# Optimization experiments

Measured on AMD Instinct MI355X. Metric: run time of the kernel, lower is better.

The kernel has to match this reference:

```python
import jax, jax.numpy as jnp
import numpy as np

B, S, H = 2, 2048, 1024
NH, HD = 16, 64
WIN = 256
EPS = 1e-5


def _layernorm(x, g, b):
    # normalize over last dim (head_dim)
    m = jnp.mean(x, axis=-1, keepdims=True)
    v = jnp.mean((x - m) ** 2, axis=-1, keepdims=True)
    return (x - m) * jax.lax.rsqrt(v + EPS) * g + b


def setup_inputs() -> dict:
    key = jax.random.key(0)
    ks = jax.random.split(key, 6)
    scale = 1.0 / np.sqrt(2.0 * H)  # ~ xavier_uniform with gain 1/sqrt(2)
    inp = {
        "x": jax.random.normal(ks[0], (B, S, H), dtype=jnp.float32),
        "Wq": jax.random.normal(ks[1], (H, H), dtype=jnp.float32) * scale,
        "bq": jnp.zeros((H,), jnp.float32),
        "Wk": jax.random.normal(ks[2], (H, H), dtype=jnp.float32) * scale,
        "bk": jnp.zeros((H,), jnp.float32),
        "Wv": jax.random.normal(ks[3], (H, H), dtype=jnp.float32) * scale,
        "bv": jnp.zeros((H,), jnp.float32),
        "Wo": jax.random.normal(ks[4], (H, H), dtype=jnp.float32) * scale,
        "bo": jnp.zeros((H,), jnp.float32),
        "ln_q_w": jnp.ones((HD,), jnp.float32),
        "ln_q_b": jnp.zeros((HD,), jnp.float32),
        "ln_k_w": jnp.ones((HD,), jnp.float32),
        "ln_k_b": jnp.zeros((HD,), jnp.float32),
    }
    return inp


def reference(x, Wq, bq, Wk, bk, Wv, bv, Wo, bo, ln_q_w, ln_q_b, ln_k_w, ln_k_b):
    b, s, _ = x.shape
    # projections (torch Linear: x @ W.T + b)
    q = (x @ Wq.T + bq).reshape(b, s, NH, HD)
    k = (x @ Wk.T + bk).reshape(b, s, NH, HD)
    v = (x @ Wv.T + bv).reshape(b, s, NH, HD)
    # QK layernorm over head_dim
    q = _layernorm(q, ln_q_w, ln_q_b)
    k = _layernorm(k, ln_k_w, ln_k_b)
    # scores [b, h, s, s]
    scores = jnp.einsum("bqhd,bkhd->bhqk", q, k) / np.sqrt(HD).astype(np.float32)
    i = jnp.arange(s)[:, None]
    j = jnp.arange(s)[None, :]
    mask = (j <= i) & (i - j <= WIN)
    scores = jnp.where(mask[None, None], scores, -jnp.inf)
    probs = jax.nn.softmax(scores, axis=-1)
    out = jnp.einsum("bhqk,bkhd->bqhd", probs, v).reshape(b, s, NH * HD)
    return out @ Wo.T + bo
```

## Files before the change

### kernel.cpp

```cpp
#include <hip/hip_runtime.h>
#include <hip/hip_bf16.h>
#include <cstdint>

typedef __hip_bfloat16 bf16;
typedef __attribute__((ext_vector_type(8))) short s16x8;
typedef __attribute__((ext_vector_type(4))) float f32x4;

#define NB_B 2
#define NB_S 2048
#define NB_H 1024
#define NB_NH 16
#define NB_HD 64
#define NB_WIN 256
#define NTOK 4096

static __device__ __forceinline__ unsigned pack_bf16(float a, float b) {
    bf16 ta = __float2bfloat16(a), tb = __float2bfloat16(b);
    return (unsigned)*(unsigned short*)&ta | ((unsigned)*(unsigned short*)&tb << 16);
}
static __device__ __forceinline__ unsigned short bf16u(float a) {
    bf16 t = __float2bfloat16(a);
    return *(unsigned short*)&t;
}

#define VMCNT(n) asm volatile("s_waitcnt vmcnt(" #n ")" ::: "memory")
#define SBAR __builtin_amdgcn_s_barrier()
#define LGKM0 do { asm volatile("s_waitcnt lgkmcnt(0)" ::: "memory"); \
                   __builtin_amdgcn_sched_barrier(0); } while (0)

__global__ void k_castall(const float* __restrict__ x, const float* __restrict__ Wq,
                          const float* __restrict__ Wk, const float* __restrict__ Wv,
                          const float* __restrict__ Wo,
                          bf16* __restrict__ xb, bf16* __restrict__ wqkvb,
                          bf16* __restrict__ wob) {
    int idx = blockIdx.x * blockDim.x + threadIdx.x;
    const float* in; bf16* out; int i;
    if (idx < 1048576)        { in = x;  out = xb;              i = idx * 4; }
    else if (idx < 1310720)   { in = Wq; out = wqkvb;           i = (idx - 1048576) * 4; }
    else if (idx < 1572864)   { in = Wk; out = wqkvb + 1048576; i = (idx - 1310720) * 4; }
    else if (idx < 1835008)   { in = Wv; out = wqkvb + 2097152; i = (idx - 1572864) * 4; }
    else                      { in = Wo; out = wob;             i = (idx - 1835008) * 4; }
    const float4 v = *(const float4*)(in + i);
    ushort4 u;
    u.x = bf16u(v.x); u.y = bf16u(v.y); u.z = bf16u(v.z); u.w = bf16u(v.w);
    *(ushort4*)((unsigned short*)out + i) = u;
}

#define GQ_STAGE(AD, BD, KT)                                                         \
    do {                                                                             \
        _Pragma("unroll")                                                            \
        for (int it_ = 0; it_ < 2; ++it_) {                                          \
            int c_ = it_ * 256 + tid;                                                \
            int row_ = c_ >> 2, pc_ = c_ & 3;                                        \
            int col_ = (pc_ ^ ((row_ >> 1) & 3)) << 3;                               \
            __builtin_amdgcn_global_load_lds(                                        \
                (const __attribute__((address_space(1))) void*)(Ap + (size_t)(m0 + row_) * 1024 + (KT) + col_), \
                (__attribute__((address_space(3))) void*)((AD) + c_ * 8), 16, 0, 0); \
            __builtin_amdgcn_global_load_lds(                                        \
                (const __attribute__((address_space(1))) void*)(Bp + (size_t)(n0 + row_) * 1024 + (KT) + col_), \
                (__attribute__((address_space(3))) void*)((BD) + c_ * 8), 16, 0, 0); \
        }                                                                            \
        __builtin_amdgcn_sched_barrier(0);                                           \
    } while (0)

#define GQ_COMPUTE(AS, BS)                                                           \
    do {                                                                             \
        const int chv_ = (g ^ ((q >> 1) & 3)) << 3;                                  \
        s16x8 af_[4], bf_[4];                                                        \
        _Pragma("unroll")                                                            \
        for (int mi_ = 0; mi_ < 4; ++mi_)                                            \
            af_[mi_] = *(const s16x8*)&(AS)[(wr * 64 + mi_ * 16 + q) * 32 + chv_];   \
        _Pragma("unroll")                                                            \
        for (int ni_ = 0; ni_ < 4; ++ni_)                                            \
            bf_[ni_] = *(const s16x8*)&(BS)[(wc * 64 + ni_ * 16 + q) * 32 + chv_];   \
        LGKM0;                                                                       \
        __builtin_amdgcn_s_setprio(1);                                               \
        _Pragma("unroll")                                                            \
        for (int mi_ = 0; mi_ < 4; ++mi_)                                            \
            _Pragma("unroll")                                                        \
            for (int ni_ = 0; ni_ < 4; ++ni_)                                        \
                acc[mi_][ni_] = __builtin_amdgcn_mfma_f32_16x16x32_bf16(             \
                    af_[mi_], bf_[ni_], acc[mi_][ni_], 0, 0, 0);                     \
        __builtin_amdgcn_s_setprio(0);                                               \
    } while (0)

#define GQ_MAINLOOP(NT)                                                              \
    GQ_STAGE(Asb + 0 * ABUF, Bsb + 0 * BBUF, 0);                                     \
    GQ_STAGE(Asb + 1 * ABUF, Bsb + 1 * BBUF, 32);                                    \
    {                                                                                \
        int bc_ = 0, bs_ = 2;                                                        \
        for (int t_ = 0; t_ < (NT) - 2; ++t_) {                                      \
            GQ_STAGE(Asb + bs_ * ABUF, Bsb + bs_ * BBUF, (t_ + 2) * 32);             \
            VMCNT(8); SBAR;                                                          \
            GQ_COMPUTE(Asb + bc_ * ABUF, Bsb + bc_ * BBUF);                          \
            SBAR;                                                                    \
            bc_ = (bc_ + 1 == 3) ? 0 : bc_ + 1;                                      \
            bs_ = (bs_ + 1 == 3) ? 0 : bs_ + 1;                                      \
        }                                                                            \
        VMCNT(4); SBAR;                                                              \
        GQ_COMPUTE(Asb + bc_ * ABUF, Bsb + bc_ * BBUF);                              \
        SBAR;                                                                        \
        bc_ = (bc_ + 1 == 3) ? 0 : bc_ + 1;                                          \
        VMCNT(0); SBAR;                                                              \
        GQ_COMPUTE(Asb + bc_ * ABUF, Bsb + bc_ * BBUF);                              \
    }

__global__ __launch_bounds__(256, 3) void k_gemm_qkv(const bf16* __restrict__ Ap,
                                                  const bf16* __restrict__ Bp,
                                                  const float* __restrict__ bq,
                                                  const float* __restrict__ bk,
                                                  const float* __restrict__ bv,
                                                  const float* __restrict__ lqw,
                                                  const float* __restrict__ lqb,
                                                  const float* __restrict__ lkw,
                                                  const float* __restrict__ lkb,
                                                  bf16* __restrict__ qbuf,
                                                  bf16* __restrict__ kbuf,
                                                  bf16* __restrict__ vtb) {
    const int ABUF = 128 * 32, BBUF = 128 * 32;
    __shared__ bf16 Asb[3 * 128 * 32];
    __shared__ bf16 Bsb[3 * 128 * 32];
    const int tid = threadIdx.x;
    const int lane = tid & 63;
    const int w = tid >> 6;
    const int wr = w >> 1, wc = w & 1;

    const int orig = blockIdx.y * gridDim.x + blockIdx.x;
    const int wk = (orig & 7) * 96 + (orig >> 3);
    const int m0 = (wk / 24) * 128, n0 = (wk % 24) * 128;

    const int g = lane >> 4, q = lane & 15;

    f32x4 acc[4][4] = {};

    GQ_MAINLOOP(32);

    const int col0 = n0 + wc * 64;
    const int hh = col0 >> 6;
    const int csub = col0 & 1023;
    const float* bias = (hh < 16) ? bq : (hh < 32) ? bk : bv;

    float bcol[4];
#pragma unroll
    for (int ni = 0; ni < 4; ++ni) bcol[ni] = bias[csub + ni * 16 + q];
#pragma unroll
    for (int mi = 0; mi < 4; ++mi)
#pragma unroll
        for (int ni = 0; ni < 4; ++ni)
#pragma unroll
            for (int r = 0; r < 4; ++r) acc[mi][ni][r] += bcol[ni];

    if (hh < 32) {
        const float* gwa = (hh < 16) ? lqw : lkw;
        const float* gba = (hh < 16) ? lqb : lkb;
        float gam[4], bet[4];
#pragma unroll
        for (int ni = 0; ni < 4; ++ni) {
            gam[ni] = gwa[ni * 16 + q];
            bet[ni] = gba[ni * 16 + q];
        }
        bf16* outp = (hh < 16) ? qbuf : kbuf;
#pragma unroll
        for (int mi = 0; mi < 4; ++mi)
#pragma unroll
            for (int r = 0; r < 4; ++r) {
                float s1 = acc[mi][0][r] + acc[mi][1][r] + acc[mi][2][r] + acc[mi][3][r];
                float s2 = acc[mi][0][r] * acc[mi][0][r] + acc[mi][1][r] * acc[mi][1][r]
                         + acc[mi][2][r] * acc[mi][2][r] + acc[mi][3][r] * acc[mi][3][r];
#pragma unroll
                for (int mm = 1; mm < 16; mm <<= 1) {
                    s1 += __shfl_xor(s1, mm, 64);
                    s2 += __shfl_xor(s2, mm, 64);
                }
                float mean = s1 * (1.f / 64.f);
                float var = s2 * (1.f / 64.f) - mean * mean;
                float rs = rsqrtf(var + 1e-5f);
                int token = m0 + wr * 64 + mi * 16 + g * 4 + r;
#pragma unroll
                for (int ni = 0; ni < 4; ++ni) {
                    float y = (acc[mi][ni][r] - mean) * rs * gam[ni] + bet[ni];
                    outp[(size_t)token * 1024 + csub + ni * 16 + q] = __float2bfloat16(y);
                }
            }
    } else {
        const int b = m0 >> 11;
        const int bh = b * 16 + (csub >> 6);
        const int sbase0 = (m0 & 2047) + wr * 64 + g * 4;
#pragma unroll
        for (int mi = 0; mi < 4; ++mi) {
            const int sb = sbase0 + mi * 16;
#pragma unroll
            for (int ni = 0; ni < 4; ++ni) {
                const int d = ni * 16 + q;
                ushort4 u;
                u.x = bf16u(acc[mi][ni][0]); u.y = bf16u(acc[mi][ni][1]);
                u.z = bf16u(acc[mi][ni][2]); u.w = bf16u(acc[mi][ni][3]);
                *(ushort4*)(vtb + ((size_t)bh * 64 + d) * 2048 + sb) = u;
            }
        }
    }
}

#define GO_STAGE(AD, BD, KT)                                                         \
    do {                                                                             \
        _Pragma("unroll")                                                            \
        for (int it_ = 0; it_ < 2; ++it_) {                                          \
            int c_ = it_ * 256 + tid;                                                \
            int row_ = c_ >> 2, pc_ = c_ & 3;                                        \
            int col_ = (pc_ ^ ((row_ >> 1) & 3)) << 3;                               \
            __builtin_amdgcn_global_load_lds(                                        \
                (const __attribute__((address_space(1))) void*)(Ap + (size_t)(m0 + row_) * 1024 + (KT) + col_), \
                (__attribute__((address_space(3))) void*)((AD) + c_ * 8), 16, 0, 0); \
        }                                                                            \
        {                                                                            \
            int row_ = tid >> 2, pc_ = tid & 3;                                      \
            int col_ = (pc_ ^ ((row_ >> 1) & 3)) << 3;                               \
            __builtin_amdgcn_global_load_lds(                                        \
                (const __attribute__((address_space(1))) void*)(Bp + (size_t)(n0 + row_) * 1024 + (KT) + col_), \
                (__attribute__((address_space(3))) void*)((BD) + tid * 8), 16, 0, 0); \
        }                                                                            \
        __builtin_amdgcn_sched_barrier(0);                                           \
    } while (0)

#define GO_COMPUTE(AS, BS)                                                           \
    do {                                                                             \
        const int chv_ = (g ^ ((q >> 1) & 3)) << 3;                                  \
        s16x8 af_[4], bf_[2];                                                        \
        _Pragma("unroll")                                                            \
        for (int mi_ = 0; mi_ < 4; ++mi_)                                            \
            af_[mi_] = *(const s16x8*)&(AS)[(wr * 64 + mi_ * 16 + q) * 32 + chv_];   \
        _Pragma("unroll")                                                            \
        for (int ni_ = 0; ni_ < 2; ++ni_)                                            \
            bf_[ni_] = *(const s16x8*)&(BS)[(wc * 32 + ni_ * 16 + q) * 32 + chv_];   \
        LGKM0;                                                                       \
        __builtin_amdgcn_s_setprio(1);                                               \
        _Pragma("unroll")                                                            \
        for (int mi_ = 0; mi_ < 4; ++mi_)                                            \
            _Pragma("unroll")                                                        \
            for (int ni_ = 0; ni_ < 2; ++ni_)                                        \
                acc[mi_][ni_] = __builtin_amdgcn_mfma_f32_16x16x32_bf16(             \
                    af_[mi_], bf_[ni_], acc[mi_][ni_], 0, 0, 0);                     \
        __builtin_amdgcn_s_setprio(0);                                               \
    } while (0)

#define GO_MAINLOOP(NT)                                                              \
    GO_STAGE(Asb + 0 * ABUF, Bsb + 0 * BBUF, 0);                                     \
    GO_STAGE(Asb + 1 * ABUF, Bsb + 1 * BBUF, 32);                                    \
    {                                                                                \
        int bc_ = 0, bs_ = 2;                                                        \
        for (int t_ = 0; t_ < (NT) - 2; ++t_) {                                      \
            GO_STAGE(Asb + bs_ * ABUF, Bsb + bs_ * BBUF, (t_ + 2) * 32);             \
            VMCNT(6); SBAR;                                                          \
            GO_COMPUTE(Asb + bc_ * ABUF, Bsb + bc_ * BBUF);                          \
            SBAR;                                                                    \
            bc_ = (bc_ + 1 == 3) ? 0 : bc_ + 1;                                      \
            bs_ = (bs_ + 1 == 3) ? 0 : bs_ + 1;                                      \
        }                                                                            \
        VMCNT(3); SBAR;                                                              \
        GO_COMPUTE(Asb + bc_ * ABUF, Bsb + bc_ * BBUF);                              \
        SBAR;                                                                        \
        bc_ = (bc_ + 1 == 3) ? 0 : bc_ + 1;                                          \
        VMCNT(0); SBAR;                                                              \
        GO_COMPUTE(Asb + bc_ * ABUF, Bsb + bc_ * BBUF);                              \
    }

__global__ __launch_bounds__(256, 4) void k_gemm_out(const bf16* __restrict__ Ap,
                                                  const bf16* __restrict__ Bp,
                                                  const float* __restrict__ bias,
                                                  float* __restrict__ Cv) {
    const int ABUF = 128 * 32, BBUF = 64 * 32;
    __shared__ bf16 Asb[3 * 128 * 32];
    __shared__ bf16 Bsb[3 * 64 * 32];
    const int tid = threadIdx.x;
    const int lane = tid & 63;
    const int w = tid >> 6;
    const int wr = w >> 1, wc = w & 1;

    const int orig = blockIdx.y * gridDim.x + blockIdx.x;
    const int wk = (orig & 7) * 64 + (orig >> 3);
    const int m0 = (wk / 16) * 128, n0 = (wk % 16) * 64;

    const int g = lane >> 4, q = lane & 15;

    f32x4 acc[4][2] = {};

    GO_MAINLOOP(32);

#pragma unroll
    for (int mi = 0; mi < 4; ++mi)
#pragma unroll
        for (int ni = 0; ni < 2; ++ni) {
            int colg = n0 + wc * 32 + ni * 16 + q;
            float bcol = bias[colg];
#pragma unroll
            for (int r = 0; r < 4; ++r) {
                int rowg = m0 + wr * 64 + mi * 16 + g * 4 + r;
                Cv[(size_t)rowg * 1024 + colg] = acc[mi][ni][r] + bcol;
            }
        }
}

#undef GQ_STAGE
#undef GQ_COMPUTE
#undef GQ_MAINLOOP
#undef GO_STAGE
#undef GO_COMPUTE
#undef GO_MAINLOOP

__global__ __launch_bounds__(256) void k_attn(const bf16* __restrict__ qb,
                                              const bf16* __restrict__ kb,
                                              const bf16* __restrict__ vt,
                                              bf16* __restrict__ att) {
    __shared__ bf16 Ks[2][32 * 64];
    __shared__ bf16 Vs[2][64 * 32];

    const int orig = blockIdx.y * gridDim.x + blockIdx.x;
    const int wk = (orig & 7) * 128 + (orig >> 3);
    const int q0 = (wk & 31) * 64;
    const int bh = wk >> 5;

    const int b = bh >> 4, h = bh & 15;
    const int tid = threadIdx.x;
    const int w = tid >> 6;
    const int lane = tid & 63;
    const int g = lane >> 4, qi = lane & 15;
    const int qw0 = q0 + w * 16;
    const int iq = qw0 + qi;

    const size_t qbase = ((size_t)(b * 2048 + iq)) * 1024 + h * 64 + g * 8;
    s16x8 bq0 = *(const s16x8*)(qb + qbase);
    s16x8 bq1 = *(const s16x8*)(qb + qbase + 32);

    f32x4 o[4] = {};
    float lp = 0.f;

    int jmin = q0 - NB_WIN; if (jmin < 0) jmin = 0;
    const int c0 = jmin >> 5;
    const int c1 = (q0 + 63) >> 5;

    const int krow = tid >> 3, kpc = tid & 7;
    const int kcol = ((kpc ^ (krow & 7)) << 3);
    const int vrow = tid >> 2, vpc = tid & 3;
    const int vcol = ((vpc ^ (vrow & 3)) << 3);
    const bf16* kbase = kb + ((size_t)(b * 2048 + krow)) * 1024 + h * 64 + kcol;
    const bf16* vbase = vt + ((size_t)bh * 64 + vrow) * 2048 + vcol;

    __builtin_amdgcn_global_load_lds(
        (const __attribute__((address_space(1))) void*)(kbase + (size_t)(c0 * 32) * 1024),
        (__attribute__((address_space(3))) void*)(&Ks[0][tid * 8]), 16, 0, 0);
    __builtin_amdgcn_global_load_lds(
        (const __attribute__((address_space(1))) void*)(vbase + c0 * 32),
        (__attribute__((address_space(3))) void*)(&Vs[0][tid * 8]), 16, 0, 0);

    int buf = 0;
    for (int c = c0; c <= c1; ++c) {
        const int ks = c * 32;
        if (c < c1) {
            const int ksn = ks + 32;
            __builtin_amdgcn_global_load_lds(
                (const __attribute__((address_space(1))) void*)(kbase + (size_t)ksn * 1024),
                (__attribute__((address_space(3))) void*)(&Ks[buf ^ 1][tid * 8]), 16, 0, 0);
            __builtin_amdgcn_global_load_lds(
                (const __attribute__((address_space(1))) void*)(vbase + ksn),
                (__attribute__((address_space(3))) void*)(&Vs[buf ^ 1][tid * 8]), 16, 0, 0);
            __builtin_amdgcn_sched_barrier(0);
            VMCNT(2);
        } else {
            VMCNT(0);
        }
        SBAR;

        if (ks + 31 >= qw0 - NB_WIN && ks <= qw0 + 15) {
            const int ch0 = ((g ^ (qi & 7)) << 3);
            const bf16* kr0 = &Ks[buf][qi * 64];
            const bf16* kr1 = &Ks[buf][(16 + qi) * 64];
            s16x8 a00 = *(const s16x8*)(kr0 + ch0);
            s16x8 a01 = *(const s16x8*)(kr0 + (ch0 ^ 32));
            s16x8 a10 = *(const s16x8*)(kr1 + ch0);
            s16x8 a11 = *(const s16x8*)(kr1 + (ch0 ^ 32));

            f32x4 s0 = {}, s1 = {};
            s0 = __builtin_amdgcn_mfma_f32_16x16x32_bf16(a00, bq0, s0, 0, 0, 0);
            s0 = __builtin_amdgcn_mfma_f32_16x16x32_bf16(a01, bq1, s0, 0, 0, 0);
            s1 = __builtin_amdgcn_mfma_f32_16x16x32_bf16(a10, bq0, s1, 0, 0, 0);
            s1 = __builtin_amdgcn_mfma_f32_16x16x32_bf16(a11, bq1, s1, 0, 0, 0);

            float p0[4], p1[4];
#pragma unroll
            for (int r = 0; r < 4; ++r) {
                int j0 = ks + 4 * g + r, j1 = j0 + 16;
                p0[r] = ((unsigned)(iq - j0) <= (unsigned)NB_WIN)
                            ? __expf(s0[r] * 0.125f - 8.f) : 0.f;
                p1[r] = ((unsigned)(iq - j1) <= (unsigned)NB_WIN)
                            ? __expf(s1[r] * 0.125f - 8.f) : 0.f;
                lp += p0[r] + p1[r];
            }
            unsigned P0 = pack_bf16(p0[0], p0[1]), P1 = pack_bf16(p0[2], p0[3]);
            unsigned Q0 = pack_bf16(p1[0], p1[1]), Q1 = pack_bf16(p1[2], p1[3]);

            const int srcA = qi + (g & 1) * 32;
            const int srcB = srcA + 16;
            unsigned tP0a = __shfl((int)P0, srcA, 64), tQ0a = __shfl((int)Q0, srcA, 64);
            unsigned tP1a = __shfl((int)P1, srcA, 64), tQ1a = __shfl((int)Q1, srcA, 64);
            unsigned tP0b = __shfl((int)P0, srcB, 64), tQ0b = __shfl((int)Q0, srcB, 64);
            unsigned tP1b = __shfl((int)P1, srcB, 64), tQ1b = __shfl((int)Q1, srcB, 64);
            union { s16x8 v; unsigned u[4]; } pa;
            pa.u[0] = (g < 2) ? tP0a : tQ0a;
            pa.u[1] = (g < 2) ? tP1a : tQ1a;
            pa.u[2] = (g < 2) ? tP0b : tQ0b;
            pa.u[3] = (g < 2) ? tP1b : tQ1b;

            const int chv = ((g ^ (qi & 3)) << 3);
#pragma unroll
            for (int db = 0; db < 4; ++db) {
                s16x8 bv = *(const s16x8*)&Vs[buf][(db * 16 + qi) * 32 + chv];
                o[db] = __builtin_amdgcn_mfma_f32_16x16x32_bf16(pa.v, bv, o[db], 0, 0, 0);
            }
        }

        SBAR;
        buf ^= 1;
    }

    float l2 = lp + __shfl_xor(lp, 16, 64);
    float lf = l2 + __shfl_xor(l2, 32, 64);
    float lr[4];
#pragma unroll
    for (int r = 0; r < 4; ++r) lr[r] = __shfl(lf, 4 * g + r, 64);

#pragma unroll
    for (int db = 0; db < 4; ++db)
#pragma unroll
        for (int r = 0; r < 4; ++r) {
            float vlu = o[db][r] / lr[r];
            att[((size_t)(b * 2048 + qw0 + 4 * g + r)) * 1024 + h * 64 + db * 16 + qi] =
                __float2bfloat16(vlu);
        }
}

extern "C" void kernel_launch(void* const* d_in, const int* in_sizes, int n_in,
                              void* d_out, int out_size, void* d_ws, size_t ws_size,
                              hipStream_t stream) {
    const float* x   = (const float*)d_in[0];
    const float* Wq  = (const float*)d_in[1];
    const float* bq  = (const float*)d_in[2];
    const float* Wk  = (const float*)d_in[3];
    const float* bk  = (const float*)d_in[4];
    const float* Wv  = (const float*)d_in[5];
    const float* bv  = (const float*)d_in[6];
    const float* Wo  = (const float*)d_in[7];
    const float* bo  = (const float*)d_in[8];
    const float* lqw = (const float*)d_in[9];
    const float* lqb = (const float*)d_in[10];
    const float* lkw = (const float*)d_in[11];
    const float* lkb = (const float*)d_in[12];

    char* ws = (char*)d_ws;
    bf16* xb    = (bf16*)(ws + 0);
    bf16* wqkvb = (bf16*)(ws + 8388608);
    bf16* wob   = (bf16*)(ws + 14680064);
    bf16* qbuf  = (bf16*)(ws + 16777216);
    bf16* kbuf  = (bf16*)(ws + 25165824);
    bf16* vtb   = (bf16*)(ws + 33554432);
    bf16* attb  = (bf16*)(ws + 41943040);

    k_castall<<<8192, 256, 0, stream>>>(x, Wq, Wk, Wv, Wo, xb, wqkvb, wob);

    k_gemm_qkv<<<dim3(24, 32), 256, 0, stream>>>(xb, wqkvb, bq, bk, bv,
                                                 lqw, lqb, lkw, lkb,
                                                 qbuf, kbuf, vtb);

    k_attn<<<dim3(32, 32), 256, 0, stream>>>(qbuf, kbuf, vtb, attb);

    k_gemm_out<<<dim3(16, 32), 256, 0, stream>>>(attb, wob, bo, (float*)d_out);
}
```

Baseline: 90.74 us.

## Deepen GEMM and attention pipelines to four LDS buffers with one barrier per step

```diff
diff --git a/kernel.cpp b/kernel.cpp
--- a/kernel.cpp
+++ b/kernel.cpp
@@ -84,28 +84,27 @@
         __builtin_amdgcn_s_setprio(0);                                               \
     } while (0)
 
-#define GQ_MAINLOOP(NT)                                                              \
+#define GQ_MAINLOOP                                                                  \
     GQ_STAGE(Asb + 0 * ABUF, Bsb + 0 * BBUF, 0);                                     \
     GQ_STAGE(Asb + 1 * ABUF, Bsb + 1 * BBUF, 32);                                    \
+    GQ_STAGE(Asb + 2 * ABUF, Bsb + 2 * BBUF, 64);                                    \
+    VMCNT(8); SBAR;                                                                  \
     {                                                                                \
-        int bc_ = 0, bs_ = 2;                                                        \
-        for (int t_ = 0; t_ < (NT) - 2; ++t_) {                                      \
-            GQ_STAGE(Asb + bs_ * ABUF, Bsb + bs_ * BBUF, (t_ + 2) * 32);             \
+        int bc_ = 0, bs_ = 3;                                                        \
+        for (int t_ = 0; t_ < 29; ++t_) {                                            \
+            GQ_COMPUTE(Asb + bc_ * ABUF, Bsb + bc_ * BBUF);                          \
+            GQ_STAGE(Asb + bs_ * ABUF, Bsb + bs_ * BBUF, (t_ + 3) * 32);             \
             VMCNT(8); SBAR;                                                          \
-            GQ_COMPUTE(Asb + bc_ * ABUF, Bsb + bc_ * BBUF);                          \
-            SBAR;                                                                    \
-            bc_ = (bc_ + 1 == 3) ? 0 : bc_ + 1;                                      \
-            bs_ = (bs_ + 1 == 3) ? 0 : bs_ + 1;                                      \
+            bc_ = (bc_ + 1) & 3; bs_ = (bs_ + 1) & 3;                                \
         }                                                                            \
+        GQ_COMPUTE(Asb + 1 * ABUF, Bsb + 1 * BBUF);                        \
         VMCNT(4); SBAR;                                                              \
-        GQ_COMPUTE(Asb + bc_ * ABUF, Bsb + bc_ * BBUF);                              \
-        SBAR;                                                                        \
-        bc_ = (bc_ + 1 == 3) ? 0 : bc_ + 1;                                          \
+        GQ_COMPUTE(Asb + 2 * ABUF, Bsb + 2 * BBUF);                        \
         VMCNT(0); SBAR;                                                              \
-        GQ_COMPUTE(Asb + bc_ * ABUF, Bsb + bc_ * BBUF);                              \
+        GQ_COMPUTE(Asb + 3 * ABUF, Bsb + 3 * BBUF);                        \
     }
 
-__global__ __launch_bounds__(256, 3) void k_gemm_qkv(const bf16* __restrict__ Ap,
+__global__ __launch_bounds__(256, 2) void k_gemm_qkv(const bf16* __restrict__ Ap,
                                                   const bf16* __restrict__ Bp,
                                                   const float* __restrict__ bq,
                                                   const float* __restrict__ bk,
@@ -118,8 +117,8 @@
                                                   bf16* __restrict__ kbuf,
                                                   bf16* __restrict__ vtb) {
     const int ABUF = 128 * 32, BBUF = 128 * 32;
-    __shared__ bf16 Asb[3 * 128 * 32];
-    __shared__ bf16 Bsb[3 * 128 * 32];
+    __shared__ bf16 Asb[4 * 128 * 32];
+    __shared__ bf16 Bsb[4 * 128 * 32];
     const int tid = threadIdx.x;
     const int lane = tid & 63;
     const int w = tid >> 6;
@@ -133,7 +132,7 @@
 
     f32x4 acc[4][4] = {};
 
-    GQ_MAINLOOP(32);
+    GQ_MAINLOOP;
 
     const int col0 = n0 + wc * 64;
     const int hh = col0 >> 6;
@@ -243,34 +242,33 @@
         __builtin_amdgcn_s_setprio(0);                                               \
     } while (0)
 
-#define GO_MAINLOOP(NT)                                                              \
+#define GO_MAINLOOP                                                                  \
     GO_STAGE(Asb + 0 * ABUF, Bsb + 0 * BBUF, 0);                                     \
     GO_STAGE(Asb + 1 * ABUF, Bsb + 1 * BBUF, 32);                                    \
+    GO_STAGE(Asb + 2 * ABUF, Bsb + 2 * BBUF, 64);                                    \
+    VMCNT(6); SBAR;                                                                  \
     {                                                                                \
-        int bc_ = 0, bs_ = 2;                                                        \
-        for (int t_ = 0; t_ < (NT) - 2; ++t_) {                                      \
-            GO_STAGE(Asb + bs_ * ABUF, Bsb + bs_ * BBUF, (t_ + 2) * 32);             \
+        int bc_ = 0, bs_ = 3;                                                        \
+        for (int t_ = 0; t_ < 29; ++t_) {                                            \
+            GO_COMPUTE(Asb + bc_ * ABUF, Bsb + bc_ * BBUF);                          \
+            GO_STAGE(Asb + bs_ * ABUF, Bsb + bs_ * BBUF, (t_ + 3) * 32);             \
             VMCNT(6); SBAR;                                                          \
-            GO_COMPUTE(Asb + bc_ * ABUF, Bsb + bc_ * BBUF);                          \
-            SBAR;                                                                    \
-            bc_ = (bc_ + 1 == 3) ? 0 : bc_ + 1;                                      \
-            bs_ = (bs_ + 1 == 3) ? 0 : bs_ + 1;                                      \
+            bc_ = (bc_ + 1) & 3; bs_ = (bs_ + 1) & 3;                                \
         }                                                                            \
+        GO_COMPUTE(Asb + 1 * ABUF, Bsb + 1 * BBUF);                        \
         VMCNT(3); SBAR;                                                              \
-        GO_COMPUTE(Asb + bc_ * ABUF, Bsb + bc_ * BBUF);                              \
-        SBAR;                                                                        \
-        bc_ = (bc_ + 1 == 3) ? 0 : bc_ + 1;                                          \
+        GO_COMPUTE(Asb + 2 * ABUF, Bsb + 2 * BBUF);                        \
         VMCNT(0); SBAR;                                                              \
-        GO_COMPUTE(Asb + bc_ * ABUF, Bsb + bc_ * BBUF);                              \
+        GO_COMPUTE(Asb + 3 * ABUF, Bsb + 3 * BBUF);                        \
     }
 
-__global__ __launch_bounds__(256, 4) void k_gemm_out(const bf16* __restrict__ Ap,
+__global__ __launch_bounds__(256, 2) void k_gemm_out(const bf16* __restrict__ Ap,
                                                   const bf16* __restrict__ Bp,
                                                   const float* __restrict__ bias,
                                                   float* __restrict__ Cv) {
     const int ABUF = 128 * 32, BBUF = 64 * 32;
-    __shared__ bf16 Asb[3 * 128 * 32];
-    __shared__ bf16 Bsb[3 * 64 * 32];
+    __shared__ bf16 Asb[4 * 128 * 32];
+    __shared__ bf16 Bsb[4 * 64 * 32];
     const int tid = threadIdx.x;
     const int lane = tid & 63;
     const int w = tid >> 6;
@@ -284,7 +282,7 @@
 
     f32x4 acc[4][2] = {};
 
-    GO_MAINLOOP(32);
+    GO_MAINLOOP;
 
 #pragma unroll
     for (int mi = 0; mi < 4; ++mi)
@@ -311,8 +309,8 @@
                                               const bf16* __restrict__ kb,
                                               const bf16* __restrict__ vt,
                                               bf16* __restrict__ att) {
-    __shared__ bf16 Ks[2][32 * 64];
-    __shared__ bf16 Vs[2][64 * 32];
+    __shared__ bf16 Ks[4][32 * 64];
+    __shared__ bf16 Vs[4][64 * 32];
 
     const int orig = blockIdx.y * gridDim.x + blockIdx.x;
     const int wk = (orig & 7) * 128 + (orig >> 3);
@@ -345,31 +343,32 @@
     const bf16* kbase = kb + ((size_t)(b * 2048 + krow)) * 1024 + h * 64 + kcol;
     const bf16* vbase = vt + ((size_t)bh * 64 + vrow) * 2048 + vcol;
 
-    __builtin_amdgcn_global_load_lds(
-        (const __attribute__((address_space(1))) void*)(kbase + (size_t)(c0 * 32) * 1024),
-        (__attribute__((address_space(3))) void*)(&Ks[0][tid * 8]), 16, 0, 0);
-    __builtin_amdgcn_global_load_lds(
-        (const __attribute__((address_space(1))) void*)(vbase + c0 * 32),
-        (__attribute__((address_space(3))) void*)(&Vs[0][tid * 8]), 16, 0, 0);
-
-    int buf = 0;
+#define ATTN_STAGE(C)                                                                \
+    do {                                                                             \
+        const int bf_ = (C) & 3;                                                     \
+        __builtin_amdgcn_global_load_lds(                                            \
+            (const __attribute__((address_space(1))) void*)(kbase + (size_t)((C) * 32) * 1024), \
+            (__attribute__((address_space(3))) void*)(&Ks[bf_][tid * 8]), 16, 0, 0); \
+        __builtin_amdgcn_global_load_lds(                                            \
+            (const __attribute__((address_space(1))) void*)(vbase + (C) * 32),       \
+            (__attribute__((address_space(3))) void*)(&Vs[bf_][tid * 8]), 16, 0, 0); \
+        __builtin_amdgcn_sched_barrier(0);                                           \
+    } while (0)
+
+    int staged = c0 + 2; if (staged > c1) staged = c1;
+    ATTN_STAGE(c0);
+    if (c0 + 1 <= c1) ATTN_STAGE(c0 + 1);
+    if (c0 + 2 <= c1) ATTN_STAGE(c0 + 2);
+
     for (int c = c0; c <= c1; ++c) {
+        const int ahead = staged - c;
+        if (ahead >= 2)      { VMCNT(4); }
+        else if (ahead == 1) { VMCNT(2); }
+        else                 { VMCNT(0); }
+        SBAR;
+
         const int ks = c * 32;
-        if (c < c1) {
-            const int ksn = ks + 32;
-            __builtin_amdgcn_global_load_lds(
-                (const __attribute__((address_space(1))) void*)(kbase + (size_t)ksn * 1024),
-                (__attribute__((address_space(3))) void*)(&Ks[buf ^ 1][tid * 8]), 16, 0, 0);
-            __builtin_amdgcn_global_load_lds(
-                (const __attribute__((address_space(1))) void*)(vbase + ksn),
-                (__attribute__((address_space(3))) void*)(&Vs[buf ^ 1][tid * 8]), 16, 0, 0);
-            __builtin_amdgcn_sched_barrier(0);
-            VMCNT(2);
-        } else {
-            VMCNT(0);
-        }
-        SBAR;
-
+        const int buf = c & 3;
         if (ks + 31 >= qw0 - NB_WIN && ks <= qw0 + 15) {
             const int ch0 = ((g ^ (qi & 7)) << 3);
             const bf16* kr0 = &Ks[buf][qi * 64];
@@ -418,9 +417,9 @@
             }
         }
 
-        SBAR;
-        buf ^= 1;
+        if (staged < c1) { ++staged; ATTN_STAGE(staged); }
     }
+#undef ATTN_STAGE
 
     float l2 = lp + __shfl_xor(lp, 16, 64);
     float lf = l2 + __shfl_xor(l2, 32, 64);
```

Measured after the change: 93.73 us. 3.3% more time.
